# Kernel tuning notes

Hardware: AMD Instinct MI355X
Metric: run time of the kernel (lower is better)

## Reference

```python
import jax, jax.numpy as jnp
import numpy as np

BATCH, LENGTH, DIM = 2, 2048, 1024
DIM_HIDDEN, NUM_HEAD = 1024, 8
BASE_LR, BASE_WD = 0.01, 0.01


def setup_inputs() -> dict:
    key = jax.random.key(0)
    ks = jax.random.split(key, 8)
    s = jnp.float32(0.02)  # init scale for linear weights
    f32 = jnp.float32
    return {
        "x": jax.random.normal(ks[0], (BATCH, LENGTH, DIM), f32),
        "hidden": jax.random.normal(ks[1], (BATCH, DIM, DIM_HIDDEN), f32),
        "log_base_lr": jnp.full((NUM_HEAD,), float(np.log(BASE_LR)), f32),
        "fc_lr_w": jax.random.normal(ks[2], (DIM, NUM_HEAD), f32) * s,
        "fc_lr_b": jnp.zeros((NUM_HEAD,), f32),
        "log_base_wd": jnp.full((NUM_HEAD,), float(np.log(BASE_WD)), f32),
        "fc_wd_w": jax.random.normal(ks[3], (DIM, NUM_HEAD), f32) * s,
        "fc_wd_b": jnp.zeros((NUM_HEAD,), f32),
        "wq": jax.random.normal(ks[4], (DIM, DIM_HIDDEN), f32) * s,
        "bq": jnp.zeros((DIM_HIDDEN,), f32),
        "wk": jax.random.normal(ks[5], (DIM, DIM_HIDDEN), f32) * s,
        "bk": jnp.zeros((DIM_HIDDEN,), f32),
        "wv": jax.random.normal(ks[6], (DIM, DIM), f32) * s,
        "bv": jnp.zeros((DIM,), f32),
    }


def reference(x, hidden, log_base_lr, fc_lr_w, fc_lr_b, log_base_wd, fc_wd_w, fc_wd_b, wq, bq, wk, bk, wv, bv):
    b, L, dim = x.shape
    n = log_base_lr.shape[0]
    dim_hidden = wq.shape[1]
    dh = dim_hidden // n

    W_prev = hidden.reshape(b, dim, n, dh).transpose(0, 2, 1, 3)          # [b,n,dim,h]
    q = (x @ wq + bq).reshape(b, L, n, dh).transpose(0, 2, 1, 3)          # [b,n,L,h]
    k = (x @ wk + bk).reshape(b, L, n, dh).transpose(0, 2, 1, 3)          # [b,n,L,h]
    v = x @ wv + bv                                                        # [b,L,dim]

    lr = (jnp.exp(log_base_lr) * jax.nn.sigmoid(x @ fc_lr_w + fc_lr_b)).transpose(0, 2, 1)   # [b,n,L]
    lwd = jnp.log1p(-jnp.exp(log_base_wd) * jax.nn.sigmoid(x @ fc_wd_w + fc_wd_b)).transpose(0, 2, 1)  # [b,n,L]

    wd_cross = jnp.exp(jnp.cumsum(lwd, axis=2))                            # [b,n,L]
    # einops.repeat 'b n l -> b n m l' then triu(1), cumsum over m, exp, triu
    rep = jnp.broadcast_to(lwd[:, :, None, :], (b, n, L, L))               # [b,n,m,l]
    wd_inner = jnp.triu(jnp.exp(jnp.cumsum(jnp.triu(rep, 1), axis=2)))     # [b,n,L,L]

    kq = jnp.einsum('bnld,bnmd->bnlm', k, q)                               # [b,n,L,L]
    mask_kq = kq * wd_inner

    WpK_V = jnp.einsum('bndh,bnlh->bnld', W_prev, k) - v[:, None]          # [b,n,L,dim]

    y_inner = -jnp.einsum('bnld,bnl,bnlm->bmd', WpK_V, lr, mask_kq)        # [b,L,dim]
    y_cross = jnp.einsum('bndh,bnlh,bnl->bld', W_prev, q, wd_cross)        # [b,L,dim]
    y = y_inner + y_cross

    Wn_inner = -jnp.einsum('bnld,bnl,bnlh->bndh', WpK_V, lr * wd_inner[:, :, :, -1], k)
    Wn_cross = W_prev * wd_cross[:, :, -1][:, :, None, None]
    W_next = (Wn_inner + Wn_cross).transpose(0, 2, 1, 3).reshape(b, dim, dim_hidden)
    return (y, W_next)
```

## Files before the change

kernel.cpp:

```cpp
#include <hip/hip_runtime.h>
#include <stdint.h>


typedef __bf16 bf16x8 __attribute__((ext_vector_type(8)));
typedef float f32x4 __attribute__((ext_vector_type(4)));
typedef unsigned short u16;
typedef u16 u16x4 __attribute__((ext_vector_type(4)));

#define MFMA16 __builtin_amdgcn_mfma_f32_16x16x32_bf16

static __device__ __forceinline__ u16 f2b(float f) {
  union { float f; uint32_t u; } v; v.f = f;
  uint32_t r = v.u + 0x7FFFu + ((v.u >> 16) & 1u);
  return (u16)(r >> 16);
}
static __device__ __forceinline__ float b2f(u16 h) {
  union { uint32_t u; float f; } v; v.u = ((uint32_t)h) << 16;
  return v.f;
}

typedef __attribute__((address_space(1))) void gvoid_t;
typedef __attribute__((address_space(3))) void lvoid_t;
static __device__ __forceinline__ void gld16(const u16* g, u16* l) {
  __builtin_amdgcn_global_load_lds((gvoid_t*)(uintptr_t)g, (lvoid_t*)l, 16, 0, 0);
}
static __device__ __forceinline__ void stage(u16* lds, const u16* __restrict__ g, int ld, int t) {
  const int r0 = t >> 2, c0 = (t & 3) << 3;
  gld16(g + (size_t)r0 * ld + c0, lds + (r0 << 5) + c0);
  gld16(g + (size_t)(r0 + 64) * ld + c0, lds + ((r0 + 64) << 5) + c0);
}

#define TILE_IDS                                   \
  const int t = threadIdx.x;                       \
  const int w = t >> 6, ln = t & 63;               \
  const int wr = (w >> 1) << 6, wc = (w & 1) << 6; \
  const int q = ln >> 4, q8 = q << 3, r = ln & 15;

static __device__ __forceinline__ void mfma_tile(const u16* As, const u16* Bs,
                                                 int wr, int wc, int q8, int r, f32x4 acc[4][4]) {
  bf16x8 af[4], bf[4];
#pragma unroll
  for (int s = 0; s < 4; ++s) af[s] = *(const bf16x8*)(As + ((wr + s * 16 + r) << 5) + q8);
#pragma unroll
  for (int s = 0; s < 4; ++s) bf[s] = *(const bf16x8*)(Bs + ((wc + s * 16 + r) << 5) + q8);
#pragma unroll
  for (int sm = 0; sm < 4; ++sm)
#pragma unroll
    for (int sn = 0; sn < 4; ++sn)
      acc[sm][sn] = MFMA16(af[sm], bf[sn], acc[sm][sn], 0, 0, 0);
}


__global__ __launch_bounds__(256) void k_cast(const float* __restrict__ s, u16* __restrict__ d) {
  const size_t i = ((size_t)blockIdx.x * 256 + threadIdx.x) * 4;
  f32x4 v = *(const f32x4*)(s + i);
  u16x4 o;
#pragma unroll
  for (int j = 0; j < 4; ++j) o[j] = f2b(v[j]);
  *(u16x4*)(d + i) = o;
}

__global__ __launch_bounds__(256) void k_zero(float* __restrict__ p) {
  const size_t i = ((size_t)blockIdx.x * 256 + threadIdx.x) * 4;
  *(f32x4*)(p + i) = f32x4{0.f, 0.f, 0.f, 0.f};
}

__global__ __launch_bounds__(256) void k_wninit(const float* __restrict__ hidden,
                                                const float* __restrict__ wdc,
                                                float* __restrict__ out2) {
  const size_t i = ((size_t)blockIdx.x * 256 + threadIdx.x) * 4;
  const int b = (int)(i >> 20);
  const int hd = (int)(i & 1023);
  const float wdcl = wdc[((size_t)(b * 8 + (hd >> 7))) * 2048 + 2047];
  f32x4 v = *(const f32x4*)(hidden + i);
  v *= wdcl;
  *(f32x4*)(out2 + i) = v;
}

__global__ __launch_bounds__(256) void k_twt(const float* __restrict__ wq, const float* __restrict__ wk,
                                             const float* __restrict__ wv, u16* __restrict__ wqT,
                                             u16* __restrict__ wkT, u16* __restrict__ wvT) {
  const int z = blockIdx.z;
  const float* src = z == 0 ? wq : z == 1 ? wk : wv;
  u16* dst = z == 0 ? wqT : z == 1 ? wkT : wvT;
  __shared__ float tile[32][33];
  const int k0 = blockIdx.x * 32, n0 = blockIdx.y * 32;
  const int tx = threadIdx.x, ty = threadIdx.y;
#pragma unroll
  for (int i = 0; i < 4; ++i)
    tile[ty + i * 8][tx] = src[(size_t)(k0 + ty + i * 8) * 1024 + n0 + tx];
  __syncthreads();
#pragma unroll
  for (int i = 0; i < 4; ++i)
    dst[(size_t)(n0 + ty + i * 8) * 1024 + k0 + tx] = f2b(tile[tx][ty + i * 8]);
}

__global__ __launch_bounds__(256) void k_lrwd(const float* __restrict__ x,
    const float* __restrict__ wlr, const float* __restrict__ blr,
    const float* __restrict__ wwd, const float* __restrict__ bwd,
    const float* __restrict__ lbl, const float* __restrict__ lbw,
    float* __restrict__ lr, float* __restrict__ lwd) {
  const int row = blockIdx.x;
  const int t = threadIdx.x;
  float pl[8] = {}, pw[8] = {};
  const float* xr = x + (size_t)row * 1024;
  for (int i = t; i < 1024; i += 256) {
    const float xv = xr[i];
    const float* wl = wlr + (size_t)i * 8;
    const float* ww = wwd + (size_t)i * 8;
#pragma unroll
    for (int j = 0; j < 8; ++j) { pl[j] += xv * wl[j]; pw[j] += xv * ww[j]; }
  }
  __shared__ float red[256][17];
#pragma unroll
  for (int j = 0; j < 8; ++j) { red[t][j] = pl[j]; red[t][j + 8] = pw[j]; }
  __syncthreads();
  for (int s = 128; s > 0; s >>= 1) {
    if (t < s) {
#pragma unroll
      for (int j = 0; j < 16; ++j) red[t][j] += red[t + s][j];
    }
    __syncthreads();
  }
  const int b = row >> 11, l = row & 2047;
  if (t < 8) {
    const float sig = 1.f / (1.f + expf(-(red[0][t] + blr[t])));
    lr[((size_t)b * 8 + t) * 2048 + l] = expf(lbl[t]) * sig;
  } else if (t < 16) {
    const int j = t - 8;
    const float sig = 1.f / (1.f + expf(-(red[0][t] + bwd[j])));
    lwd[((size_t)b * 8 + j) * 2048 + l] = log1pf(-expf(lbw[j]) * sig);
  }
}

__global__ __launch_bounds__(256) void k_scan(const float* __restrict__ lwd,
                                              float* __restrict__ wdc, float* __restrict__ wdlast) {
  const int bn = blockIdx.x, t = threadIdx.x;
  const float* src = lwd + (size_t)bn * 2048;
  float v[8], s = 0.f;
#pragma unroll
  for (int i = 0; i < 8; ++i) { v[i] = src[t * 8 + i]; s += v[i]; }
  __shared__ float ps[256];
  ps[t] = s;
  __syncthreads();
  for (int off = 1; off < 256; off <<= 1) {
    const float add = (t >= off) ? ps[t - off] : 0.f;
    __syncthreads();
    ps[t] += add;
    __syncthreads();
  }
  float run = ps[t] - s;
  const float lwd_last = src[2047];
  float* wo = wdc + (size_t)bn * 2048;
  float* wl = wdlast + (size_t)bn * 2048;
#pragma unroll
  for (int i = 0; i < 8; ++i) {
    run += v[i];
    const int idx = t * 8 + i;
    wo[idx] = expf(run);
    const int c = (idx + 1 < 2047) ? (idx + 1) : 2047;
    wl[idx] = expf(lwd_last * (float)c);
  }
}

__global__ __launch_bounds__(256) void k_qs(u16* __restrict__ qb, const float* __restrict__ wdc) {
  const size_t base = ((size_t)blockIdx.x * 256 + threadIdx.x) * 4;
  const int b = (int)(base >> 21);
  const int rem = (int)(base & 2097151);
  const int m = rem >> 10, hd = rem & 1023;
  const float sc = wdc[((size_t)b * 8 + (hd >> 7)) * 2048 + m];
  u16x4 v = *(const u16x4*)(qb + base);
#pragma unroll
  for (int j = 0; j < 4; ++j) v[j] = f2b(b2f(v[j]) * sc);
  *(u16x4*)(qb + base) = v;
}


__global__ __launch_bounds__(256) void g_qk(const u16* __restrict__ xb, const u16* __restrict__ wqT,
    const u16* __restrict__ wkT, const float* __restrict__ bq, const float* __restrict__ bk,
    u16* __restrict__ qb, u16* __restrict__ kb) {
  __shared__ u16 As[4096], Bs[4096];
  TILE_IDS
  const int m0 = blockIdx.x * 128, n0 = blockIdx.y * 128, z = blockIdx.z;
  const u16* A = xb + (size_t)m0 * 1024;
  const u16* B = (z ? wkT : wqT) + (size_t)n0 * 1024;
  const float* bias = z ? bk : bq;
  u16* outp = z ? kb : qb;
  f32x4 acc[4][4] = {};
  for (int k0 = 0; k0 < 1024; k0 += 32) {
    __syncthreads();
    stage(As, A + k0, 1024, t);
    stage(Bs, B + k0, 1024, t);
    __syncthreads();
    mfma_tile(As, Bs, wr, wc, q8, r, acc);
  }
#pragma unroll
  for (int sn = 0; sn < 4; ++sn) {
    const int col = n0 + wc + sn * 16 + r;
    const float bc = bias[col];
#pragma unroll
    for (int sm = 0; sm < 4; ++sm)
#pragma unroll
      for (int i = 0; i < 4; ++i) {
        const int gm = m0 + wr + sm * 16 + (q << 2) + i;
        outp[(size_t)gm * 1024 + col] = f2b(acc[sm][sn][i] + bc);
      }
  }
}

__global__ __launch_bounds__(256) void g_vtkt(const u16* __restrict__ xb, const u16* __restrict__ wvT,
    const u16* __restrict__ wkT, const float* __restrict__ bv, const float* __restrict__ bk,
    const float* __restrict__ wdl, u16* __restrict__ vT, u16* __restrict__ kTw) {
  __shared__ u16 As[4096], Bs[4096];
  TILE_IDS
  const int m0 = blockIdx.x * 128, l0 = blockIdx.y * 128;
  const int sel = blockIdx.z >> 1, b = blockIdx.z & 1;
  const u16* A = (sel ? wkT : wvT) + (size_t)m0 * 1024;
  const u16* B = xb + ((size_t)(b * 2048 + l0)) * 1024;
  f32x4 acc[4][4] = {};
  for (int k0 = 0; k0 < 1024; k0 += 32) {
    __syncthreads();
    stage(As, A + k0, 1024, t);
    stage(Bs, B + k0, 1024, t);
    __syncthreads();
    mfma_tile(As, Bs, wr, wc, q8, r, acc);
  }
#pragma unroll
  for (int sm = 0; sm < 4; ++sm)
#pragma unroll
    for (int i = 0; i < 4; ++i) {
      const int row = m0 + wr + sm * 16 + (q << 2) + i;
      const float bc = sel ? bk[row] : bv[row];
#pragma unroll
      for (int sn = 0; sn < 4; ++sn) {
        const int l = l0 + wc + sn * 16 + r;
        const float v = acc[sm][sn][i] + bc;
        if (!sel) {
          vT[((size_t)(b * 1024 + row)) * 2048 + l] = f2b(v);
        } else {
          const int n = row >> 7;
          kTw[((size_t)(b * 1024 + row)) * 2048 + l] =
              f2b(v * wdl[((size_t)(b * 8 + n)) * 2048 + l]);
        }
      }
    }
}

__global__ __launch_bounds__(256) void g2_s(const u16* __restrict__ qb, const u16* __restrict__ kb,
                                            const float* __restrict__ lwd, u16* __restrict__ S) {
  const int p = blockIdx.x, bn = blockIdx.y, b = bn >> 3, n = bn & 7;
  int mi = (int)((sqrtf(8.f * p + 1.f) - 1.f) * 0.5f);
  while ((mi + 1) * (mi + 2) / 2 <= p) ++mi;
  while (mi * (mi + 1) / 2 > p) --mi;
  const int li = p - mi * (mi + 1) / 2;
  const int m0 = mi * 128, l0 = li * 128;
  __shared__ u16 As[4096], Bs[4096];
  TILE_IDS
  const u16* A = qb + ((size_t)(b * 2048 + m0)) * 1024 + n * 128;
  const u16* B = kb + ((size_t)(b * 2048 + l0)) * 1024 + n * 128;
  f32x4 acc[4][4] = {};
  for (int k0 = 0; k0 < 128; k0 += 32) {
    __syncthreads();
    stage(As, A + k0, 1024, t);
    stage(Bs, B + k0, 1024, t);
    __syncthreads();
    mfma_tile(As, Bs, wr, wc, q8, r, acc);
  }
  const float* lwdp = lwd + (size_t)bn * 2048;
  u16* Sp = S + (size_t)bn * 2048 * 2048;
#pragma unroll
  for (int sm = 0; sm < 4; ++sm)
#pragma unroll
    for (int i = 0; i < 4; ++i) {
      const int m = m0 + wr + sm * 16 + (q << 2) + i;
      const float lm = lwdp[m];
#pragma unroll
      for (int sn = 0; sn < 4; ++sn) {
        const int l = l0 + wc + sn * 16 + r;
        float v = 0.f;
        if (l <= m) {
          const float c = (l == m) ? (float)m : (float)(l + 1);
          v = -acc[sm][sn][i] * __expf(lm * c);
        }
        Sp[(size_t)m * 2048 + l] = f2b(v);
      }
    }
}

__global__ __launch_bounds__(256) void g3_af(const u16* __restrict__ hb, const u16* __restrict__ kb,
                                             const u16* __restrict__ vT, const float* __restrict__ lr,
                                             u16* __restrict__ AfT) {
  const int d0 = blockIdx.x * 128, l0 = blockIdx.y * 128;
  const int bn = blockIdx.z, b = bn >> 3, n = bn & 7;
  __shared__ u16 As[4096], Bs[4096];
  TILE_IDS
  const u16* A = hb + ((size_t)(b * 1024 + d0)) * 1024 + n * 128;
  const u16* B = kb + ((size_t)(b * 2048 + l0)) * 1024 + n * 128;
  f32x4 acc[4][4] = {};
  for (int k0 = 0; k0 < 128; k0 += 32) {
    __syncthreads();
    stage(As, A + k0, 1024, t);
    stage(Bs, B + k0, 1024, t);
    __syncthreads();
    mfma_tile(As, Bs, wr, wc, q8, r, acc);
  }
  const float* lrp = lr + (size_t)bn * 2048;
#pragma unroll
  for (int sm = 0; sm < 4; ++sm)
#pragma unroll
    for (int i = 0; i < 4; ++i) {
      const int d = d0 + wr + sm * 16 + (q << 2) + i;
#pragma unroll
      for (int sn = 0; sn < 4; ++sn) {
        const int l = l0 + wc + sn * 16 + r;
        const float v = (acc[sm][sn][i] - b2f(vT[((size_t)(b * 1024 + d)) * 2048 + l])) * lrp[l];
        AfT[((size_t)bn * 1024 + d) * 2048 + l] = f2b(v);
      }
    }
}

__global__ __launch_bounds__(256) void g4(const u16* __restrict__ S, const u16* __restrict__ AfT,
                                          const u16* __restrict__ Qs, const u16* __restrict__ hb,
                                          float* __restrict__ y) {
  TILE_IDS
  const int mip = blockIdx.x, dj = blockIdx.y, z = blockIdx.z;
  const int b = z >> 3, n = z & 7;
  const int d0 = dj * 128;
  __shared__ u16 As[4096], Bs[4096];
  float* Y = y + (size_t)b * 2048 * 1024;
#pragma unroll 1
  for (int tsel = 0; tsel < 2; ++tsel) {
    const int mi = tsel ? (15 - mip) : mip;
    const int m0 = mi * 128;
    f32x4 acc[4][4] = {};
    const u16* A = S + (size_t)z * 2048 * 2048 + (size_t)m0 * 2048;
    const u16* B = AfT + ((size_t)z * 1024 + d0) * 2048;
    const int nk = 4 * mi + 4;
    for (int c = 0; c < nk; ++c) {
      const int k0 = c * 32;
      __syncthreads();
      stage(As, A + k0, 2048, t);
      stage(Bs, B + k0, 2048, t);
      __syncthreads();
      mfma_tile(As, Bs, wr, wc, q8, r, acc);
    }
    const u16* A2 = Qs + ((size_t)(b * 2048 + m0)) * 1024 + n * 128;
    const u16* B2 = hb + ((size_t)(b * 1024 + d0)) * 1024 + n * 128;
    for (int c = 0; c < 4; ++c) {
      const int k0 = c * 32;
      __syncthreads();
      stage(As, A2 + k0, 1024, t);
      stage(Bs, B2 + k0, 1024, t);
      __syncthreads();
      mfma_tile(As, Bs, wr, wc, q8, r, acc);
    }
#pragma unroll
    for (int sm = 0; sm < 4; ++sm)
#pragma unroll
      for (int i = 0; i < 4; ++i) {
        const int m = m0 + wr + sm * 16 + (q << 2) + i;
#pragma unroll
        for (int sn = 0; sn < 4; ++sn)
          atomicAdd(&Y[(size_t)m * 1024 + d0 + wc + sn * 16 + r], acc[sm][sn][i]);
      }
  }
}

__global__ __launch_bounds__(256) void g5_wn(const u16* __restrict__ AfT, const u16* __restrict__ kTw,
                                             float* __restrict__ out2) {
  const int d0 = blockIdx.x * 128, nj = blockIdx.y;
  const int z = blockIdx.z, b = z >> 2, kc = z & 3;
  const int bn = b * 8 + nj;
  __shared__ u16 As[4096], Bs[4096];
  TILE_IDS
  const u16* A = AfT + ((size_t)bn * 1024 + d0) * 2048 + kc * 512;
  const u16* B = kTw + ((size_t)(b * 1024 + nj * 128)) * 2048 + kc * 512;
  f32x4 acc[4][4] = {};
  for (int k0 = 0; k0 < 512; k0 += 32) {
    __syncthreads();
    stage(As, A + k0, 2048, t);
    stage(Bs, B + k0, 2048, t);
    __syncthreads();
    mfma_tile(As, Bs, wr, wc, q8, r, acc);
  }
#pragma unroll
  for (int sm = 0; sm < 4; ++sm)
#pragma unroll
    for (int i = 0; i < 4; ++i) {
      const int d = d0 + wr + sm * 16 + (q << 2) + i;
#pragma unroll
      for (int sn = 0; sn < 4; ++sn) {
        const int hd = nj * 128 + wc + sn * 16 + r;
        atomicAdd(&out2[((size_t)(b * 1024 + d)) * 1024 + hd], -acc[sm][sn][i]);
      }
    }
}


extern "C" void kernel_launch(void* const* d_in, const int* in_sizes, int n_in,
                              void* d_out, int out_size, void* d_ws, size_t ws_size,
                              hipStream_t stream) {
  const float* x      = (const float*)d_in[0];
  const float* hidden = (const float*)d_in[1];
  const float* lbl    = (const float*)d_in[2];
  const float* wlr    = (const float*)d_in[3];
  const float* blr    = (const float*)d_in[4];
  const float* lbw    = (const float*)d_in[5];
  const float* wwd    = (const float*)d_in[6];
  const float* bwd    = (const float*)d_in[7];
  const float* wq     = (const float*)d_in[8];
  const float* bq     = (const float*)d_in[9];
  const float* wk     = (const float*)d_in[10];
  const float* bk     = (const float*)d_in[11];
  const float* wv     = (const float*)d_in[12];
  const float* bv     = (const float*)d_in[13];
  float* out = (float*)d_out;

  char* ws = (char*)d_ws;
  const size_t MB = 1u << 20;
  u16* S     = (u16*)(ws);
  u16* xb    = (u16*)(ws);
  u16* wqT   = (u16*)(ws + 8 * MB);
  u16* wkT   = (u16*)(ws + 10 * MB);
  u16* wvT   = (u16*)(ws + 12 * MB);
  u16* AfT   = (u16*)(ws + 128 * MB);
  u16* hb    = (u16*)(ws + 192 * MB);
  u16* qb    = (u16*)(ws + 196 * MB);
  u16* kb    = (u16*)(ws + 204 * MB);
  u16* kTw   = (u16*)(ws + 212 * MB);
  u16* vT    = (u16*)(ws + 220 * MB);
  float* lr  = (float*)(ws + 228 * MB);
  float* lwd = (float*)(ws + 228 * MB + 131072);
  float* wdc = (float*)(ws + 228 * MB + 262144);
  float* wdl = (float*)(ws + 228 * MB + 393216);
  (void)ws_size; (void)n_in; (void)in_sizes; (void)out_size;

  const size_t YSZ = (size_t)2 * 2048 * 1024;

  k_cast<<<4096, 256, 0, stream>>>(x, xb);
  k_cast<<<2048, 256, 0, stream>>>(hidden, hb);
  k_twt<<<dim3(32, 32, 3), dim3(32, 8), 0, stream>>>(wq, wk, wv, wqT, wkT, wvT);
  k_lrwd<<<4096, 256, 0, stream>>>(x, wlr, blr, wwd, bwd, lbl, lbw, lr, lwd);
  k_scan<<<16, 256, 0, stream>>>(lwd, wdc, wdl);
  g_qk<<<dim3(32, 8, 2), 256, 0, stream>>>(xb, wqT, wkT, bq, bk, qb, kb);
  g_vtkt<<<dim3(8, 16, 4), 256, 0, stream>>>(xb, wvT, wkT, bv, bk, wdl, vT, kTw);
  g2_s<<<dim3(136, 16), 256, 0, stream>>>(qb, kb, lwd, S);
  k_qs<<<4096, 256, 0, stream>>>(qb, wdc);
  g3_af<<<dim3(8, 16, 16), 256, 0, stream>>>(hb, kb, vT, lr, AfT);
  k_zero<<<4096, 256, 0, stream>>>(out);
  k_wninit<<<2048, 256, 0, stream>>>(hidden, wdc, out + YSZ);
  g4<<<dim3(8, 8, 16), 256, 0, stream>>>(S, AfT, qb, hb, out);
  g5_wn<<<dim3(8, 8, 8), 256, 0, stream>>>(AfT, kTw, out + YSZ);
}
```

Baseline: 506.9 us.

## Merge independent kernels into fused multi-role launches and double the GEMM K-step

Independent stages are packed into single launches that dispatch on block index: casts, weight transposes and lr/wd projections go into one prep kernel; the QK and VT/KT GEMMs into one; the S, AfT, zeroing and W init into one; the y and W_next GEMMs into one. Every GEMM now stages 64-wide K slices (two 32-wide halves) per barrier pair, halving sync count but doubling LDS per block. The aim is to cut launch overhead and fill the GPU better by running small independent grids concurrently. The larger LDS footprint may lower occupancy.

Result: faster. 431.0 us (-15.0%).

```diff
diff --git a/kernel.cpp b/kernel.cpp
--- a/kernel.cpp
+++ b/kernel.cpp
@@ -24,10 +24,17 @@
 static __device__ __forceinline__ void gld16(const u16* g, u16* l) {
   __builtin_amdgcn_global_load_lds((gvoid_t*)(uintptr_t)g, (lvoid_t*)l, 16, 0, 0);
 }
-static __device__ __forceinline__ void stage(u16* lds, const u16* __restrict__ g, int ld, int t) {
+
+static __device__ __forceinline__ void stage64(u16* lds, const u16* __restrict__ g, int ld, int t) {
   const int r0 = t >> 2, c0 = (t & 3) << 3;
-  gld16(g + (size_t)r0 * ld + c0, lds + (r0 << 5) + c0);
-  gld16(g + (size_t)(r0 + 64) * ld + c0, lds + ((r0 + 64) << 5) + c0);
+  const u16* ga = g + (size_t)r0 * ld + c0;
+  const u16* gb = g + (size_t)(r0 + 64) * ld + c0;
+  u16* la = lds + (r0 << 5) + c0;
+  u16* lb = lds + ((r0 + 64) << 5) + c0;
+  gld16(ga, la);
+  gld16(gb, lb);
+  gld16(ga + 32, la + 4096);
+  gld16(gb + 32, lb + 4096);
 }
 
 #define TILE_IDS                                   \
@@ -36,102 +43,112 @@
   const int wr = (w >> 1) << 6, wc = (w & 1) << 6; \
   const int q = ln >> 4, q8 = q << 3, r = ln & 15;
 
-static __device__ __forceinline__ void mfma_tile(const u16* As, const u16* Bs,
-                                                 int wr, int wc, int q8, int r, f32x4 acc[4][4]) {
-  bf16x8 af[4], bf[4];
-#pragma unroll
-  for (int s = 0; s < 4; ++s) af[s] = *(const bf16x8*)(As + ((wr + s * 16 + r) << 5) + q8);
-#pragma unroll
-  for (int s = 0; s < 4; ++s) bf[s] = *(const bf16x8*)(Bs + ((wc + s * 16 + r) << 5) + q8);
-#pragma unroll
-  for (int sm = 0; sm < 4; ++sm)
-#pragma unroll
-    for (int sn = 0; sn < 4; ++sn)
-      acc[sm][sn] = MFMA16(af[sm], bf[sn], acc[sm][sn], 0, 0, 0);
-}
-
-
-__global__ __launch_bounds__(256) void k_cast(const float* __restrict__ s, u16* __restrict__ d) {
-  const size_t i = ((size_t)blockIdx.x * 256 + threadIdx.x) * 4;
-  f32x4 v = *(const f32x4*)(s + i);
-  u16x4 o;
-#pragma unroll
-  for (int j = 0; j < 4; ++j) o[j] = f2b(v[j]);
-  *(u16x4*)(d + i) = o;
-}
-
-__global__ __launch_bounds__(256) void k_zero(float* __restrict__ p) {
-  const size_t i = ((size_t)blockIdx.x * 256 + threadIdx.x) * 4;
-  *(f32x4*)(p + i) = f32x4{0.f, 0.f, 0.f, 0.f};
-}
-
-__global__ __launch_bounds__(256) void k_wninit(const float* __restrict__ hidden,
-                                                const float* __restrict__ wdc,
-                                                float* __restrict__ out2) {
-  const size_t i = ((size_t)blockIdx.x * 256 + threadIdx.x) * 4;
-  const int b = (int)(i >> 20);
-  const int hd = (int)(i & 1023);
-  const float wdcl = wdc[((size_t)(b * 8 + (hd >> 7))) * 2048 + 2047];
-  f32x4 v = *(const f32x4*)(hidden + i);
-  v *= wdcl;
-  *(f32x4*)(out2 + i) = v;
-}
-
-__global__ __launch_bounds__(256) void k_twt(const float* __restrict__ wq, const float* __restrict__ wk,
-                                             const float* __restrict__ wv, u16* __restrict__ wqT,
-                                             u16* __restrict__ wkT, u16* __restrict__ wvT) {
-  const int z = blockIdx.z;
-  const float* src = z == 0 ? wq : z == 1 ? wk : wv;
-  u16* dst = z == 0 ? wqT : z == 1 ? wkT : wvT;
-  __shared__ float tile[32][33];
-  const int k0 = blockIdx.x * 32, n0 = blockIdx.y * 32;
-  const int tx = threadIdx.x, ty = threadIdx.y;
-#pragma unroll
-  for (int i = 0; i < 4; ++i)
-    tile[ty + i * 8][tx] = src[(size_t)(k0 + ty + i * 8) * 1024 + n0 + tx];
-  __syncthreads();
-#pragma unroll
-  for (int i = 0; i < 4; ++i)
-    dst[(size_t)(n0 + ty + i * 8) * 1024 + k0 + tx] = f2b(tile[tx][ty + i * 8]);
-}
-
-__global__ __launch_bounds__(256) void k_lrwd(const float* __restrict__ x,
+static __device__ __forceinline__ void mfma_tile64(const u16* As, const u16* Bs,
+                                                   int wr, int wc, int q8, int r, f32x4 acc[4][4]) {
+#pragma unroll
+  for (int kk = 0; kk < 2; ++kk) {
+    const u16* Ak = As + (kk << 12);
+    const u16* Bk = Bs + (kk << 12);
+    bf16x8 af[4], bf[4];
+#pragma unroll
+    for (int s = 0; s < 4; ++s) af[s] = *(const bf16x8*)(Ak + ((wr + s * 16 + r) << 5) + q8);
+#pragma unroll
+    for (int s = 0; s < 4; ++s) bf[s] = *(const bf16x8*)(Bk + ((wc + s * 16 + r) << 5) + q8);
+#pragma unroll
+    for (int sm = 0; sm < 4; ++sm)
+#pragma unroll
+      for (int sn = 0; sn < 4; ++sn)
+        acc[sm][sn] = MFMA16(af[sm], bf[sn], acc[sm][sn], 0, 0, 0);
+  }
+}
+
+static __device__ __forceinline__ void gemm_loop(u16* As, u16* Bs,
+    const u16* __restrict__ A, int lda, const u16* __restrict__ B, int ldb, int nc,
+    int wr, int wc, int q8, int r, int t, f32x4 acc[4][4]) {
+  for (int c = 0; c < nc; ++c) {
+    __syncthreads();
+    stage64(As, A + c * 64, lda, t);
+    stage64(Bs, B + c * 64, ldb, t);
+    __syncthreads();
+    mfma_tile64(As, Bs, wr, wc, q8, r, acc);
+  }
+}
+
+
+__global__ __launch_bounds__(256) void k_prep(const float* __restrict__ x,
+    const float* __restrict__ hidden, const float* __restrict__ wq,
+    const float* __restrict__ wk, const float* __restrict__ wv,
     const float* __restrict__ wlr, const float* __restrict__ blr,
     const float* __restrict__ wwd, const float* __restrict__ bwd,
     const float* __restrict__ lbl, const float* __restrict__ lbw,
+    u16* __restrict__ xb, u16* __restrict__ hb, u16* __restrict__ wqT,
+    u16* __restrict__ wkT, u16* __restrict__ wvT,
     float* __restrict__ lr, float* __restrict__ lwd) {
-  const int row = blockIdx.x;
-  const int t = threadIdx.x;
-  float pl[8] = {}, pw[8] = {};
-  const float* xr = x + (size_t)row * 1024;
-  for (int i = t; i < 1024; i += 256) {
-    const float xv = xr[i];
-    const float* wl = wlr + (size_t)i * 8;
-    const float* ww = wwd + (size_t)i * 8;
-#pragma unroll
-    for (int j = 0; j < 8; ++j) { pl[j] += xv * wl[j]; pw[j] += xv * ww[j]; }
-  }
-  __shared__ float red[256][17];
-#pragma unroll
-  for (int j = 0; j < 8; ++j) { red[t][j] = pl[j]; red[t][j + 8] = pw[j]; }
-  __syncthreads();
-  for (int s = 128; s > 0; s >>= 1) {
-    if (t < s) {
-#pragma unroll
-      for (int j = 0; j < 16; ++j) red[t][j] += red[t + s][j];
+  __shared__ float smem[4352];
+  const int bid = blockIdx.x, t = threadIdx.x;
+  if (bid < 4096) {
+    const size_t i = ((size_t)bid * 256 + t) * 4;
+    f32x4 v = *(const f32x4*)(x + i);
+    u16x4 o;
+#pragma unroll
+    for (int j = 0; j < 4; ++j) o[j] = f2b(v[j]);
+    *(u16x4*)(xb + i) = o;
+  } else if (bid < 6144) {
+    const size_t i = ((size_t)(bid - 4096) * 256 + t) * 4;
+    f32x4 v = *(const f32x4*)(hidden + i);
+    u16x4 o;
+#pragma unroll
+    for (int j = 0; j < 4; ++j) o[j] = f2b(v[j]);
+    *(u16x4*)(hb + i) = o;
+  } else if (bid < 9216) {
+    const int idx = bid - 6144;
+    const int z = idx >> 10, rem = idx & 1023;
+    const float* src = z == 0 ? wq : z == 1 ? wk : wv;
+    u16* dst = z == 0 ? wqT : z == 1 ? wkT : wvT;
+    const int k0 = (rem >> 5) * 32, n0 = (rem & 31) * 32;
+    float (*tile)[33] = (float(*)[33])smem;
+    const int tx = t & 31, ty = t >> 5;
+#pragma unroll
+    for (int i = 0; i < 4; ++i)
+      tile[ty + i * 8][tx] = src[(size_t)(k0 + ty + i * 8) * 1024 + n0 + tx];
+    __syncthreads();
+#pragma unroll
+    for (int i = 0; i < 4; ++i)
+      dst[(size_t)(n0 + ty + i * 8) * 1024 + k0 + tx] = f2b(tile[tx][ty + i * 8]);
+  } else {
+    const int row = bid - 9216;
+    float pl[8] = {}, pw[8] = {};
+    const float* xr = x + (size_t)row * 1024;
+    for (int i = t; i < 1024; i += 256) {
+      const float xv = xr[i];
+      const float* wl = wlr + (size_t)i * 8;
+      const float* ww = wwd + (size_t)i * 8;
+#pragma unroll
+      for (int j = 0; j < 8; ++j) { pl[j] += xv * wl[j]; pw[j] += xv * ww[j]; }
     }
-    __syncthreads();
-  }
-  const int b = row >> 11, l = row & 2047;
-  if (t < 8) {
-    const float sig = 1.f / (1.f + expf(-(red[0][t] + blr[t])));
-    lr[((size_t)b * 8 + t) * 2048 + l] = expf(lbl[t]) * sig;
-  } else if (t < 16) {
-    const int j = t - 8;
-    const float sig = 1.f / (1.f + expf(-(red[0][t] + bwd[j])));
-    lwd[((size_t)b * 8 + j) * 2048 + l] = log1pf(-expf(lbw[j]) * sig);
-  }
-}
+    float (*red)[17] = (float(*)[17])smem;
+#pragma unroll
+    for (int j = 0; j < 8; ++j) { red[t][j] = pl[j]; red[t][j + 8] = pw[j]; }
+    __syncthreads();
+    for (int s = 128; s > 0; s >>= 1) {
+      if (t < s) {
+#pragma unroll
+        for (int j = 0; j < 16; ++j) red[t][j] += red[t + s][j];
+      }
+      __syncthreads();
+    }
+    const int b = row >> 11, l = row & 2047;
+    if (t < 8) {
+      const float sig = 1.f / (1.f + expf(-(red[0][t] + blr[t])));
+      lr[((size_t)b * 8 + t) * 2048 + l] = expf(lbl[t]) * sig;
+    } else if (t < 16) {
+      const int j = t - 8;
+      const float sig = 1.f / (1.f + expf(-(red[0][t] + bwd[j])));
+      lwd[((size_t)b * 8 + j) * 2048 + l] = log1pf(-expf(lbw[j]) * sig);
+    }
+  }
+}
+
 
 __global__ __launch_bounds__(256) void k_scan(const float* __restrict__ lwd,
                                               float* __restrict__ wdc, float* __restrict__ wdlast) {
@@ -162,6 +179,140 @@
     wl[idx] = expf(lwd_last * (float)c);
   }
 }
+
+
+__global__ __launch_bounds__(256) void k_qkv(const u16* __restrict__ xb,
+    const u16* __restrict__ wqT, const u16* __restrict__ wkT, const u16* __restrict__ wvT,
+    const float* __restrict__ bq, const float* __restrict__ bk, const float* __restrict__ bv,
+    const float* __restrict__ wdl,
+    u16* __restrict__ qb, u16* __restrict__ kb, u16* __restrict__ vT, u16* __restrict__ kTw) {
+  __shared__ u16 As[8192], Bs[8192];
+  TILE_IDS
+  const int bid = blockIdx.x;
+  f32x4 acc[4][4] = {};
+  if (bid < 512) {
+    const int z = bid >> 8, rem = bid & 255;
+    const int m0 = (rem >> 3) * 128, n0 = (rem & 7) * 128;
+    gemm_loop(As, Bs, xb + (size_t)m0 * 1024, 1024,
+              (z ? wkT : wqT) + (size_t)n0 * 1024, 1024, 16, wr, wc, q8, r, t, acc);
+    const float* bias = z ? bk : bq;
+    u16* outp = z ? kb : qb;
+#pragma unroll
+    for (int sn = 0; sn < 4; ++sn) {
+      const int col = n0 + wc + sn * 16 + r;
+      const float bc = bias[col];
+#pragma unroll
+      for (int sm = 0; sm < 4; ++sm)
+#pragma unroll
+        for (int i = 0; i < 4; ++i) {
+          const int gm = m0 + wr + sm * 16 + (q << 2) + i;
+          outp[(size_t)gm * 1024 + col] = f2b(acc[sm][sn][i] + bc);
+        }
+    }
+  } else {
+    const int idx = bid - 512;
+    const int zz = idx >> 7, rem = idx & 127;
+    const int sel = zz >> 1, b = zz & 1;
+    const int m0 = (rem >> 4) * 128, l0 = (rem & 15) * 128;
+    gemm_loop(As, Bs, (sel ? wkT : wvT) + (size_t)m0 * 1024, 1024,
+              xb + ((size_t)(b * 2048 + l0)) * 1024, 1024, 16, wr, wc, q8, r, t, acc);
+#pragma unroll
+    for (int sm = 0; sm < 4; ++sm)
+#pragma unroll
+      for (int i = 0; i < 4; ++i) {
+        const int row = m0 + wr + sm * 16 + (q << 2) + i;
+        const float bc = sel ? bk[row] : bv[row];
+#pragma unroll
+        for (int sn = 0; sn < 4; ++sn) {
+          const int l = l0 + wc + sn * 16 + r;
+          const float v = acc[sm][sn][i] + bc;
+          if (!sel) {
+            vT[((size_t)(b * 1024 + row)) * 2048 + l] = f2b(v);
+          } else {
+            const int n = row >> 7;
+            kTw[((size_t)(b * 1024 + row)) * 2048 + l] =
+                f2b(v * wdl[((size_t)(b * 8 + n)) * 2048 + l]);
+          }
+        }
+      }
+  }
+}
+
+
+__global__ __launch_bounds__(256) void k_mid(const u16* __restrict__ qb,
+    const u16* __restrict__ kb, const u16* __restrict__ hb, const u16* __restrict__ vT,
+    const float* __restrict__ lr, const float* __restrict__ lwd, const float* __restrict__ wdc,
+    const float* __restrict__ hidden,
+    u16* __restrict__ S, u16* __restrict__ AfT, float* __restrict__ y, float* __restrict__ out2) {
+  __shared__ u16 As[8192], Bs[8192];
+  TILE_IDS
+  const int bid = blockIdx.x;
+  if (bid < 2176) {
+    const int p = bid % 136, bn = bid / 136, b = bn >> 3, n = bn & 7;
+    int mi = (int)((sqrtf(8.f * p + 1.f) - 1.f) * 0.5f);
+    while ((mi + 1) * (mi + 2) / 2 <= p) ++mi;
+    while (mi * (mi + 1) / 2 > p) --mi;
+    const int li = p - mi * (mi + 1) / 2;
+    const int m0 = mi * 128, l0 = li * 128;
+    f32x4 acc[4][4] = {};
+    gemm_loop(As, Bs, qb + ((size_t)(b * 2048 + m0)) * 1024 + n * 128, 1024,
+              kb + ((size_t)(b * 2048 + l0)) * 1024 + n * 128, 1024, 2, wr, wc, q8, r, t, acc);
+    const float* lwdp = lwd + (size_t)bn * 2048;
+    u16* Sp = S + (size_t)bn * 2048 * 2048;
+#pragma unroll
+    for (int sm = 0; sm < 4; ++sm)
+#pragma unroll
+      for (int i = 0; i < 4; ++i) {
+        const int m = m0 + wr + sm * 16 + (q << 2) + i;
+        const float lm = lwdp[m];
+#pragma unroll
+        for (int sn = 0; sn < 4; ++sn) {
+          const int l = l0 + wc + sn * 16 + r;
+          float v = 0.f;
+          if (l <= m) {
+            const float c = (l == m) ? (float)m : (float)(l + 1);
+            v = -acc[sm][sn][i] * __expf(lm * c);
+          }
+          Sp[(size_t)m * 2048 + l] = f2b(v);
+        }
+      }
+  } else if (bid < 4224) {
+    const int idx = bid - 2176;
+    const int bn = idx >> 7, rem = idx & 127;
+    const int l0 = (rem >> 3) * 128, d0 = (rem & 7) * 128;
+    const int b = bn >> 3, n = bn & 7;
+    f32x4 acc[4][4] = {};
+    gemm_loop(As, Bs, hb + ((size_t)(b * 1024 + d0)) * 1024 + n * 128, 1024,
+              kb + ((size_t)(b * 2048 + l0)) * 1024 + n * 128, 1024, 2, wr, wc, q8, r, t, acc);
+    const float* lrp = lr + (size_t)bn * 2048;
+#pragma unroll
+    for (int sm = 0; sm < 4; ++sm)
+#pragma unroll
+      for (int i = 0; i < 4; ++i) {
+        const int d = d0 + wr + sm * 16 + (q << 2) + i;
+#pragma unroll
+        for (int sn = 0; sn < 4; ++sn) {
+          const int l = l0 + wc + sn * 16 + r;
+          const float v = (acc[sm][sn][i] - b2f(vT[((size_t)(b * 1024 + d)) * 2048 + l])) * lrp[l];
+          AfT[((size_t)bn * 1024 + d) * 2048 + l] = f2b(v);
+        }
+      }
+  } else if (bid < 5248) {
+    const size_t i = ((size_t)(bid - 4224) * 256 + t) * 16;
+#pragma unroll
+    for (int j = 0; j < 4; ++j)
+      *(f32x4*)(y + i + j * 4) = f32x4{0.f, 0.f, 0.f, 0.f};
+  } else {
+    const size_t i = ((size_t)(bid - 5248) * 256 + t) * 4;
+    const int b = (int)(i >> 20);
+    const int hd = (int)(i & 1023);
+    const float wdcl = wdc[((size_t)(b * 8 + (hd >> 7))) * 2048 + 2047];
+    f32x4 v = *(const f32x4*)(hidden + i);
+    v *= wdcl;
+    *(f32x4*)(out2 + i) = v;
+  }
+}
+
 
 __global__ __launch_bounds__(256) void k_qs(u16* __restrict__ qb, const float* __restrict__ wdc) {
   const size_t base = ((size_t)blockIdx.x * 256 + threadIdx.x) * 4;
@@ -176,224 +327,59 @@
 }
 
 
-__global__ __launch_bounds__(256) void g_qk(const u16* __restrict__ xb, const u16* __restrict__ wqT,
-    const u16* __restrict__ wkT, const float* __restrict__ bq, const float* __restrict__ bk,
-    u16* __restrict__ qb, u16* __restrict__ kb) {
-  __shared__ u16 As[4096], Bs[4096];
+__global__ __launch_bounds__(256) void k_fin(const u16* __restrict__ S,
+    const u16* __restrict__ AfT, const u16* __restrict__ Qs, const u16* __restrict__ hb,
+    const u16* __restrict__ kTw, float* __restrict__ y, float* __restrict__ out2) {
+  __shared__ u16 As[8192], Bs[8192];
   TILE_IDS
-  const int m0 = blockIdx.x * 128, n0 = blockIdx.y * 128, z = blockIdx.z;
-  const u16* A = xb + (size_t)m0 * 1024;
-  const u16* B = (z ? wkT : wqT) + (size_t)n0 * 1024;
-  const float* bias = z ? bk : bq;
-  u16* outp = z ? kb : qb;
-  f32x4 acc[4][4] = {};
-  for (int k0 = 0; k0 < 1024; k0 += 32) {
-    __syncthreads();
-    stage(As, A + k0, 1024, t);
-    stage(Bs, B + k0, 1024, t);
-    __syncthreads();
-    mfma_tile(As, Bs, wr, wc, q8, r, acc);
-  }
-#pragma unroll
-  for (int sn = 0; sn < 4; ++sn) {
-    const int col = n0 + wc + sn * 16 + r;
-    const float bc = bias[col];
+  const int bid = blockIdx.x;
+  if (bid < 1024) {
+    const int z = bid >> 6, rem = bid & 63;
+    const int mip = rem >> 3, dj = rem & 7;
+    const int b = z >> 3, n = z & 7;
+    const int d0 = dj * 128;
+    float* Y = y + (size_t)b * 2048 * 1024;
+#pragma unroll 1
+    for (int tsel = 0; tsel < 2; ++tsel) {
+      const int mi = tsel ? (15 - mip) : mip;
+      const int m0 = mi * 128;
+      f32x4 acc[4][4] = {};
+      gemm_loop(As, Bs, S + (size_t)z * 2048 * 2048 + (size_t)m0 * 2048, 2048,
+                AfT + ((size_t)z * 1024 + d0) * 2048, 2048, 2 * mi + 2, wr, wc, q8, r, t, acc);
+      gemm_loop(As, Bs, Qs + ((size_t)(b * 2048 + m0)) * 1024 + n * 128, 1024,
+                hb + ((size_t)(b * 1024 + d0)) * 1024 + n * 128, 1024, 2, wr, wc, q8, r, t, acc);
+#pragma unroll
+      for (int sm = 0; sm < 4; ++sm)
+#pragma unroll
+        for (int i = 0; i < 4; ++i) {
+          const int m = m0 + wr + sm * 16 + (q << 2) + i;
+#pragma unroll
+          for (int sn = 0; sn < 4; ++sn)
+            atomicAdd(&Y[(size_t)m * 1024 + d0 + wc + sn * 16 + r], acc[sm][sn][i]);
+        }
+    }
+  } else {
+    const int idx = bid - 1024;
+    const int z = idx >> 6, rem = idx & 63;
+    const int d0 = (rem >> 3) * 128, nj = rem & 7;
+    const int b = z >> 2, kc = z & 3;
+    const int bn = b * 8 + nj;
+    f32x4 acc[4][4] = {};
+    gemm_loop(As, Bs, AfT + ((size_t)bn * 1024 + d0) * 2048 + kc * 512, 2048,
+              kTw + ((size_t)(b * 1024 + nj * 128)) * 2048 + kc * 512, 2048, 8,
+              wr, wc, q8, r, t, acc);
 #pragma unroll
     for (int sm = 0; sm < 4; ++sm)
 #pragma unroll
       for (int i = 0; i < 4; ++i) {
-        const int gm = m0 + wr + sm * 16 + (q << 2) + i;
-        outp[(size_t)gm * 1024 + col] = f2b(acc[sm][sn][i] + bc);
+        const int d = d0 + wr + sm * 16 + (q << 2) + i;
+#pragma unroll
+        for (int sn = 0; sn < 4; ++sn) {
+          const int hd = nj * 128 + wc + sn * 16 + r;
+          atomicAdd(&out2[((size_t)(b * 1024 + d)) * 1024 + hd], -acc[sm][sn][i]);
+        }
       }
   }
-}
-
-__global__ __launch_bounds__(256) void g_vtkt(const u16* __restrict__ xb, const u16* __restrict__ wvT,
-    const u16* __restrict__ wkT, const float* __restrict__ bv, const float* __restrict__ bk,
-    const float* __restrict__ wdl, u16* __restrict__ vT, u16* __restrict__ kTw) {
-  __shared__ u16 As[4096], Bs[4096];
-  TILE_IDS
-  const int m0 = blockIdx.x * 128, l0 = blockIdx.y * 128;
-  const int sel = blockIdx.z >> 1, b = blockIdx.z & 1;
-  const u16* A = (sel ? wkT : wvT) + (size_t)m0 * 1024;
-  const u16* B = xb + ((size_t)(b * 2048 + l0)) * 1024;
-  f32x4 acc[4][4] = {};
-  for (int k0 = 0; k0 < 1024; k0 += 32) {
-    __syncthreads();
-    stage(As, A + k0, 1024, t);
-    stage(Bs, B + k0, 1024, t);
-    __syncthreads();
-    mfma_tile(As, Bs, wr, wc, q8, r, acc);
-  }
-#pragma unroll
-  for (int sm = 0; sm < 4; ++sm)
-#pragma unroll
-    for (int i = 0; i < 4; ++i) {
-      const int row = m0 + wr + sm * 16 + (q << 2) + i;
-      const float bc = sel ? bk[row] : bv[row];
-#pragma unroll
-      for (int sn = 0; sn < 4; ++sn) {
-        const int l = l0 + wc + sn * 16 + r;
-        const float v = acc[sm][sn][i] + bc;
-        if (!sel) {
-          vT[((size_t)(b * 1024 + row)) * 2048 + l] = f2b(v);
-        } else {
-          const int n = row >> 7;
-          kTw[((size_t)(b * 1024 + row)) * 2048 + l] =
-              f2b(v * wdl[((size_t)(b * 8 + n)) * 2048 + l]);
-        }
-      }
-    }
-}
-
-__global__ __launch_bounds__(256) void g2_s(const u16* __restrict__ qb, const u16* __restrict__ kb,
-                                            const float* __restrict__ lwd, u16* __restrict__ S) {
-  const int p = blockIdx.x, bn = blockIdx.y, b = bn >> 3, n = bn & 7;
-  int mi = (int)((sqrtf(8.f * p + 1.f) - 1.f) * 0.5f);
-  while ((mi + 1) * (mi + 2) / 2 <= p) ++mi;
-  while (mi * (mi + 1) / 2 > p) --mi;
-  const int li = p - mi * (mi + 1) / 2;
-  const int m0 = mi * 128, l0 = li * 128;
-  __shared__ u16 As[4096], Bs[4096];
-  TILE_IDS
-  const u16* A = qb + ((size_t)(b * 2048 + m0)) * 1024 + n * 128;
-  const u16* B = kb + ((size_t)(b * 2048 + l0)) * 1024 + n * 128;
-  f32x4 acc[4][4] = {};
-  for (int k0 = 0; k0 < 128; k0 += 32) {
-    __syncthreads();
-    stage(As, A + k0, 1024, t);
-    stage(Bs, B + k0, 1024, t);
-    __syncthreads();
-    mfma_tile(As, Bs, wr, wc, q8, r, acc);
-  }
-  const float* lwdp = lwd + (size_t)bn * 2048;
-  u16* Sp = S + (size_t)bn * 2048 * 2048;
-#pragma unroll
-  for (int sm = 0; sm < 4; ++sm)
-#pragma unroll
-    for (int i = 0; i < 4; ++i) {
-      const int m = m0 + wr + sm * 16 + (q << 2) + i;
-      const float lm = lwdp[m];
-#pragma unroll
-      for (int sn = 0; sn < 4; ++sn) {
-        const int l = l0 + wc + sn * 16 + r;
-        float v = 0.f;
-        if (l <= m) {
-          const float c = (l == m) ? (float)m : (float)(l + 1);
-          v = -acc[sm][sn][i] * __expf(lm * c);
-        }
-        Sp[(size_t)m * 2048 + l] = f2b(v);
-      }
-    }
-}
-
-__global__ __launch_bounds__(256) void g3_af(const u16* __restrict__ hb, const u16* __restrict__ kb,
-                                             const u16* __restrict__ vT, const float* __restrict__ lr,
-                                             u16* __restrict__ AfT) {
-  const int d0 = blockIdx.x * 128, l0 = blockIdx.y * 128;
-  const int bn = blockIdx.z, b = bn >> 3, n = bn & 7;
-  __shared__ u16 As[4096], Bs[4096];
-  TILE_IDS
-  const u16* A = hb + ((size_t)(b * 1024 + d0)) * 1024 + n * 128;
-  const u16* B = kb + ((size_t)(b * 2048 + l0)) * 1024 + n * 128;
-  f32x4 acc[4][4] = {};
-  for (int k0 = 0; k0 < 128; k0 += 32) {
-    __syncthreads();
-    stage(As, A + k0, 1024, t);
-    stage(Bs, B + k0, 1024, t);
-    __syncthreads();
-    mfma_tile(As, Bs, wr, wc, q8, r, acc);
-  }
-  const float* lrp = lr + (size_t)bn * 2048;
-#pragma unroll
-  for (int sm = 0; sm < 4; ++sm)
-#pragma unroll
-    for (int i = 0; i < 4; ++i) {
-      const int d = d0 + wr + sm * 16 + (q << 2) + i;
-#pragma unroll
-      for (int sn = 0; sn < 4; ++sn) {
-        const int l = l0 + wc + sn * 16 + r;
-        const float v = (acc[sm][sn][i] - b2f(vT[((size_t)(b * 1024 + d)) * 2048 + l])) * lrp[l];
-        AfT[((size_t)bn * 1024 + d) * 2048 + l] = f2b(v);
-      }
-    }
-}
-
-__global__ __launch_bounds__(256) void g4(const u16* __restrict__ S, const u16* __restrict__ AfT,
-                                          const u16* __restrict__ Qs, const u16* __restrict__ hb,
-                                          float* __restrict__ y) {
-  TILE_IDS
-  const int mip = blockIdx.x, dj = blockIdx.y, z = blockIdx.z;
-  const int b = z >> 3, n = z & 7;
-  const int d0 = dj * 128;
-  __shared__ u16 As[4096], Bs[4096];
-  float* Y = y + (size_t)b * 2048 * 1024;
-#pragma unroll 1
-  for (int tsel = 0; tsel < 2; ++tsel) {
-    const int mi = tsel ? (15 - mip) : mip;
-    const int m0 = mi * 128;
-    f32x4 acc[4][4] = {};
-    const u16* A = S + (size_t)z * 2048 * 2048 + (size_t)m0 * 2048;
-    const u16* B = AfT + ((size_t)z * 1024 + d0) * 2048;
-    const int nk = 4 * mi + 4;
-    for (int c = 0; c < nk; ++c) {
-      const int k0 = c * 32;
-      __syncthreads();
-      stage(As, A + k0, 2048, t);
-      stage(Bs, B + k0, 2048, t);
-      __syncthreads();
-      mfma_tile(As, Bs, wr, wc, q8, r, acc);
-    }
-    const u16* A2 = Qs + ((size_t)(b * 2048 + m0)) * 1024 + n * 128;
-    const u16* B2 = hb + ((size_t)(b * 1024 + d0)) * 1024 + n * 128;
-    for (int c = 0; c < 4; ++c) {
-      const int k0 = c * 32;
-      __syncthreads();
-      stage(As, A2 + k0, 1024, t);
-      stage(Bs, B2 + k0, 1024, t);
-      __syncthreads();
-      mfma_tile(As, Bs, wr, wc, q8, r, acc);
-    }
-#pragma unroll
-    for (int sm = 0; sm < 4; ++sm)
-#pragma unroll
-      for (int i = 0; i < 4; ++i) {
-        const int m = m0 + wr + sm * 16 + (q << 2) + i;
-#pragma unroll
-        for (int sn = 0; sn < 4; ++sn)
-          atomicAdd(&Y[(size_t)m * 1024 + d0 + wc + sn * 16 + r], acc[sm][sn][i]);
-      }
-  }
-}
-
-__global__ __launch_bounds__(256) void g5_wn(const u16* __restrict__ AfT, const u16* __restrict__ kTw,
-                                             float* __restrict__ out2) {
-  const int d0 = blockIdx.x * 128, nj = blockIdx.y;
-  const int z = blockIdx.z, b = z >> 2, kc = z & 3;
-  const int bn = b * 8 + nj;
-  __shared__ u16 As[4096], Bs[4096];
-  TILE_IDS
-  const u16* A = AfT + ((size_t)bn * 1024 + d0) * 2048 + kc * 512;
-  const u16* B = kTw + ((size_t)(b * 1024 + nj * 128)) * 2048 + kc * 512;
-  f32x4 acc[4][4] = {};
-  for (int k0 = 0; k0 < 512; k0 += 32) {
-    __syncthreads();
-    stage(As, A + k0, 2048, t);
-    stage(Bs, B + k0, 2048, t);
-    __syncthreads();
-    mfma_tile(As, Bs, wr, wc, q8, r, acc);
-  }
-#pragma unroll
-  for (int sm = 0; sm < 4; ++sm)
-#pragma unroll
-    for (int i = 0; i < 4; ++i) {
-      const int d = d0 + wr + sm * 16 + (q << 2) + i;
-#pragma unroll
-      for (int sn = 0; sn < 4; ++sn) {
-        const int hd = nj * 128 + wc + sn * 16 + r;
-        atomicAdd(&out2[((size_t)(b * 1024 + d)) * 1024 + hd], -acc[sm][sn][i]);
-      }
-    }
 }
 
 
@@ -437,18 +423,11 @@
 
   const size_t YSZ = (size_t)2 * 2048 * 1024;
 
-  k_cast<<<4096, 256, 0, stream>>>(x, xb);
-  k_cast<<<2048, 256, 0, stream>>>(hidden, hb);
-  k_twt<<<dim3(32, 32, 3), dim3(32, 8), 0, stream>>>(wq, wk, wv, wqT, wkT, wvT);
-  k_lrwd<<<4096, 256, 0, stream>>>(x, wlr, blr, wwd, bwd, lbl, lbw, lr, lwd);
+  k_prep<<<13312, 256, 0, stream>>>(x, hidden, wq, wk, wv, wlr, blr, wwd, bwd,
+                                    lbl, lbw, xb, hb, wqT, wkT, wvT, lr, lwd);
   k_scan<<<16, 256, 0, stream>>>(lwd, wdc, wdl);
-  g_qk<<<dim3(32, 8, 2), 256, 0, stream>>>(xb, wqT, wkT, bq, bk, qb, kb);
-  g_vtkt<<<dim3(8, 16, 4), 256, 0, stream>>>(xb, wvT, wkT, bv, bk, wdl, vT, kTw);
-  g2_s<<<dim3(136, 16), 256, 0, stream>>>(qb, kb, lwd, S);
+  k_qkv<<<1024, 256, 0, stream>>>(xb, wqT, wkT, wvT, bq, bk, bv, wdl, qb, kb, vT, kTw);
+  k_mid<<<7296, 256, 0, stream>>>(qb, kb, hb, vT, lr, lwd, wdc, hidden, S, AfT, out, out + YSZ);
   k_qs<<<4096, 256, 0, stream>>>(qb, wdc);
-  g3_af<<<dim3(8, 16, 16), 256, 0, stream>>>(hb, kb, vT, lr, AfT);
-  k_zero<<<4096, 256, 0, stream>>>(out);
-  k_wninit<<<2048, 256, 0, stream>>>(hidden, wdc, out + YSZ);
-  g4<<<dim3(8, 8, 16), 256, 0, stream>>>(S, AfT, qb, hb, out);
-  g5_wn<<<dim3(8, 8, 8), 256, 0, stream>>>(AfT, kTw, out + YSZ);
-}
+  k_fin<<<1536, 256, 0, stream>>>(S, AfT, qb, hb, kTw, out, out + YSZ);
+}
```
